# Performance work log

Measured on AMD Instinct MI355X. Metric: run time of the kernel, lower is better.

The kernel has to match this reference:

```python
import jax, jax.numpy as jnp
import numpy as np

N = 256            # state_space_size
BF = (4, 4, 4)     # branching_factors
T = 128            # time steps
D_IN = 64          # input_size
D_T = 64           # time_embedding_size
BATCH = 16
NUM_NODES = N * 4 * 4 * 4  # 16384


def setup_inputs() -> dict:
    key = jax.random.key(0)
    ks = jax.random.split(key, 20)

    def lin_w(k, out_d, in_d):
        return jax.random.normal(k, (out_d, in_d), jnp.float32) / np.sqrt(in_d)

    inp = {
        "x": jax.random.normal(ks[0], (BATCH, T, N), jnp.float32),
        "t_embeddings_schedule": jax.random.normal(ks[1], (T, D_T), jnp.float32),
        "input_vector": jax.random.normal(ks[2], (BATCH, T, D_IN), jnp.float32),
        # Fanout node params
        "Wa": lin_w(ks[3], NUM_NODES, N),
        "ba": jnp.zeros((NUM_NODES,), jnp.float32),
        "Wt": lin_w(ks[4], NUM_NODES, D_T),
        "Wi": lin_w(ks[5], NUM_NODES, D_IN),
        # Node with bf[:3]=[4,4,4]: reduces last 4 -> [N,4,4]
        "w3": jax.random.normal(ks[6], (N, 4, 4, 4), jnp.float32) * np.sqrt(2.0 / (4 + N * 16)),
        "tW3": lin_w(ks[7], N * 16, D_T),
        "tb3": jnp.zeros((N * 16,), jnp.float32),
        # Node with bf[:2]=[4,4]
        "w2": jax.random.normal(ks[8], (N, 4, 4), jnp.float32) * np.sqrt(2.0 / (4 + N * 4)),
        "tW2": lin_w(ks[9], N * 4, D_T),
        "tb2": jnp.zeros((N * 4,), jnp.float32),
        # Node with bf[:1]=[4]
        "w1": jax.random.normal(ks[10], (N, 4), jnp.float32) * np.sqrt(2.0 / (4 + N)),
        "tW1": lin_w(ks[11], N, D_T),
        "tb1": jnp.zeros((N,), jnp.float32),
    }
    return inp


def _node(act, t_emb, w, tW, tb):
    # act: [..., T, N, *bf]; w: [N, *bf]; reduce last branching dim
    tproj = (t_emb @ tW.T + tb).reshape(t_emb.shape[0], *w.shape[:-1])  # [T, N, *bf[:-1]]
    pre = (w * act).sum(-1) + tproj  # broadcast over leading batch dims
    return jax.nn.softplus(pre)


def reference(x, t_embeddings_schedule, input_vector, Wa, ba, Wt, Wi,
              w3, tW3, tb3, w2, tW2, tb2, w1, tW1, tb1):
    t_emb = t_embeddings_schedule
    # Fanout: [B, T, N] -> [B, T, N, 4, 4, 4]
    pre = x @ Wa.T + ba + (t_emb @ Wt.T) + input_vector @ Wi.T  # [B, T, NUM_NODES]
    act = jax.nn.softplus(pre.reshape(*pre.shape[:-1], N, *BF))
    # Tree: deepest node first (insert-at-1 order in original)
    act = _node(act, t_emb, w3, tW3, tb3)  # [B, T, N, 4, 4]
    act = _node(act, t_emb, w2, tW2, tb2)  # [B, T, N, 4]
    act = _node(act, t_emb, w1, tW1, tb1)  # [B, T, N]
    return act
```

## Files before the change

### kernel.cpp

```cpp
#include <hip/hip_runtime.h>

typedef __attribute__((ext_vector_type(16))) float f32x16;
typedef __attribute__((ext_vector_type(8))) __bf16 bf16x8;
typedef __attribute__((ext_vector_type(8))) unsigned short u16x8;

__device__ __forceinline__ unsigned short f2bf(float f) {
    unsigned int u = __float_as_uint(f);
    u += 0x7fffu + ((u >> 16) & 1u);
    return (unsigned short)(u >> 16);
}

__device__ __forceinline__ float softplus_f(float x) {
    float e = __expf(-fabsf(x));
    return fmaf(__log2f(1.0f + e), 0.69314718056f, fmaxf(x, 0.0f));
}

typedef __attribute__((address_space(3))) void lds_void_t;
typedef __attribute__((address_space(1))) void glb_void_t;

__device__ __forceinline__ void load16_to_lds(const void* g, const void* l) {
    __builtin_amdgcn_global_load_lds((glb_void_t*)(unsigned long long)g,
                                     (lds_void_t*)(unsigned int)(unsigned long long)l,
                                     16, 0, 0);
}

#define REPACK_NB 2
#define REPACK_BLOCKS 1728
#define TPROJ_BLOCKS 336
#define PREP_BLOCKS (REPACK_BLOCKS + TPROJ_BLOCKS)
__global__ __launch_bounds__(256) void prep(
        const float* __restrict__ x, const float* __restrict__ iv,
        const float* __restrict__ temb,
        const float* __restrict__ Wa, const float* __restrict__ Wi,
        const float* __restrict__ Wt,
        const float* __restrict__ tW3, const float* __restrict__ tb3,
        const float* __restrict__ tW2, const float* __restrict__ tb2,
        const float* __restrict__ tW1, const float* __restrict__ tb1,
        unsigned short* __restrict__ Abf ,
        float* __restrict__ tp3T, float* __restrict__ tp2T, float* __restrict__ tp1T) {
    __shared__ float se[32 * 64];
    const int tid = threadIdx.x;

    if (blockIdx.x < TPROJ_BLOCKS) {
        const int bx = blockIdx.x % 84;
        const int by = blockIdx.x / 84;
        const int tbase = by * 32;
        for (int i = tid; i < 32 * 64; i += 256) se[i] = temb[tbase * 64 + i];
        __syncthreads();
        const int j = bx * 64 + (tid >> 2);
        const float* W; const float* bias; float* outp; int jl;
        if      (j < 4096) { W = tW3; bias = tb3; outp = tp3T; jl = j; }
        else if (j < 5120) { W = tW2; bias = tb2; outp = tp2T; jl = j - 4096; }
        else               { W = tW1; bias = tb1; outp = tp1T; jl = j - 5120; }
        float4 wreg[16];
        const float4* wrow = (const float4*)(W + (size_t)jl * 64);
        #pragma unroll
        for (int k = 0; k < 16; ++k) wreg[k] = wrow[k];
        const float b = bias[jl];
        #pragma unroll
        for (int s = 0; s < 8; ++s) {
            const int tl = (tid & 3) + s * 4;
            const float4* e4 = (const float4*)&se[tl * 64];
            float a = b;
            #pragma unroll
            for (int k = 0; k < 16; ++k) {
                float4 e = e4[k];
                a += wreg[k].x * e.x + wreg[k].y * e.y + wreg[k].z * e.z + wreg[k].w * e.w;
            }
            outp[(size_t)jl * 128 + tbase + tl] = a;
        }
        return;
    }

    const int stride = REPACK_BLOCKS * 256;
    const int tid0 = (blockIdx.x - TPROJ_BLOCKS) * 256 + tid;
    float4 f[REPACK_NB][2];
    #pragma unroll
    for (int c = 0; c < REPACK_NB; ++c) {
        const int idx = tid0 + c * stride;
        const bool isA = idx < 98304;
        const int widx = isA ? idx : idx - 98304;
        const int row = widx / 48;
        const int kk  = (widx % 48) * 8;
        const float* p0 = isA ? (x    + (size_t)row * 256) : (Wa + (size_t)row * 256);
        const float* p1 = isA ? (iv   + (size_t)row * 64)  : (Wi + (size_t)row * 64);
        const float* p2 = isA ? (temb + (size_t)(row & 127) * 64) : (Wt + (size_t)row * 64);
        const float* src = (kk < 256) ? (p0 + kk) : ((kk < 320) ? (p1 + kk - 256) : (p2 + kk - 320));
        f[c][0] = ((const float4*)src)[0];
        f[c][1] = ((const float4*)src)[1];
    }
    #pragma unroll
    for (int c = 0; c < REPACK_NB; ++c) {
        const int idx = tid0 + c * stride;
        const bool isA = idx < 98304;
        const int widx = isA ? idx : idx - 98304;
        const int row = widx / 48;
        const int ch  = widx % 48;
        const size_t dst = isA ? (size_t)(((row >> 5) * 48 + ch) * 32 + (row & 31))
                               : (size_t)idx;
        u16x8 o;
        o[0] = f2bf(f[c][0].x); o[1] = f2bf(f[c][0].y); o[2] = f2bf(f[c][0].z); o[3] = f2bf(f[c][0].w);
        o[4] = f2bf(f[c][1].x); o[5] = f2bf(f[c][1].y); o[6] = f2bf(f[c][1].z); o[7] = f2bf(f[c][1].w);
        *(u16x8*)(Abf + dst * 8) = o;
    }
}

__global__ __launch_bounds__(256, 3)
void fused_gemm_tree(const unsigned short* __restrict__ Wbf,
                     const unsigned short* __restrict__ Abf,
                     const float* __restrict__ ba,
                     const float* __restrict__ tp3T, const float* __restrict__ tp2T,
                     const float* __restrict__ tp1T,
                     const float* __restrict__ w3, const float* __restrict__ w2,
                     const float* __restrict__ w1,
                     float* __restrict__ out) {
    __shared__ unsigned short sW[2][128 * 64];

    const int tid  = threadIdx.x;
    const int wave = tid >> 6;
    const int lane = tid & 63;
    const int wr = wave >> 1;
    const int wc = wave & 1;
    const int lane31 = lane & 31;
    const int h = lane >> 5;

    const int node0 = blockIdx.x * 128;
    const int m0    = blockIdx.y * 128;

    f32x16 acc[2][2];
    #pragma unroll
    for (int fm = 0; fm < 2; ++fm)
        #pragma unroll
        for (int s2 = 0; s2 < 4; ++s2) {
            const float4 b4 = *(const float4*)&ba[node0 + wr * 64 + fm * 32 + 8 * s2 + 4 * h];
            #pragma unroll
            for (int l = 0; l < 4; ++l) {
                acc[fm][0][s2 * 4 + l] = ((const float*)&b4)[l];
                acc[fm][1][s2 * 4 + l] = ((const float*)&b4)[l];
            }
        }

    const unsigned short* aBase = Wbf + (size_t)node0 * 384;
    const int wrow0 = wr * 64 + lane31;

    const int mtBase = blockIdx.y * 4 + wc * 2;
    const unsigned short* bC0 = Abf + (((size_t)(mtBase + 0) * 48 + h) * 32 + lane31) * 8;
    const unsigned short* bC1 = Abf + (((size_t)(mtBase + 1) * 48 + h) * 32 + lane31) * 8;

    int srow[4], skch[4];
    #pragma unroll
    for (int rr = 0; rr < 4; ++rr) {
        const int p = rr * 256 + tid;
        srow[rr] = p >> 3;
        skch[rr] = (p & 7) ^ (srow[rr] & 7);
    }
    #define STAGE_A(K0, BB)                                                        \
        _Pragma("unroll")                                                          \
        for (int rr = 0; rr < 4; ++rr)                                             \
            load16_to_lds(aBase + (size_t)srow[rr] * 384 + (K0) + skch[rr] * 8,    \
                          &sW[BB][(size_t)(rr * 256 + wave * 64) * 8]);

    STAGE_A(0, 0);
    __syncthreads();

    #pragma unroll
    for (int it = 0; it < 6; ++it) {
        const int k0 = it * 64;
        bf16x8 bfr[2][4];
        const int cbase = k0 >> 3;
        #pragma unroll
        for (int s = 0; s < 4; ++s) {
            bfr[0][s] = *(const bf16x8*)(bC0 + (size_t)(cbase + 2 * s) * 256);
            bfr[1][s] = *(const bf16x8*)(bC1 + (size_t)(cbase + 2 * s) * 256);
        }
        if (it < 5) { STAGE_A(k0 + 64, (it + 1) & 1); }
        #pragma unroll
        for (int s = 0; s < 4; ++s) {
            const int kc = s * 2 + h;
            const int slot = (kc ^ (lane & 7)) * 8;
            bf16x8 af[2];
            #pragma unroll
            for (int fm = 0; fm < 2; ++fm)
                af[fm] = *(const bf16x8*)&sW[it & 1][(wrow0 + fm * 32) * 64 + slot];
            acc[0][0] = __builtin_amdgcn_mfma_f32_32x32x16_bf16(af[0], bfr[0][s], acc[0][0], 0, 0, 0);
            acc[0][1] = __builtin_amdgcn_mfma_f32_32x32x16_bf16(af[0], bfr[1][s], acc[0][1], 0, 0, 0);
            acc[1][0] = __builtin_amdgcn_mfma_f32_32x32x16_bf16(af[1], bfr[0][s], acc[1][0], 0, 0, 0);
            acc[1][1] = __builtin_amdgcn_mfma_f32_32x32x16_bf16(af[1], bfr[1][s], acc[1][1], 0, 0, 0);
        }
        if (it < 5) __syncthreads();
    }

    const int n = blockIdx.x * 2 + wr;
    const int t0 = wc * 64 + lane31;

    float4 w3v[2][4];
    #pragma unroll
    for (int fm = 0; fm < 2; ++fm)
        #pragma unroll
        for (int s2 = 0; s2 < 4; ++s2)
            w3v[fm][s2] = *(const float4*)&w3[n * 64 + fm * 32 + 8 * s2 + 4 * h];

    float w2v[4][2], w1v[4];
    #pragma unroll
    for (int i = 0; i < 4; ++i) {
        #pragma unroll
        for (int s2b = 0; s2b < 2; ++s2b)
            w2v[i][s2b] = w2[n * 16 + i * 4 + 2 * s2b + h];
        w1v[i] = w1[n * 4 + i];
    }
    float tp3v[2][2][4];
    #pragma unroll
    for (int fm = 0; fm < 2; ++fm)
        #pragma unroll
        for (int cf = 0; cf < 2; ++cf) {
            const int t = t0 + cf * 32;
            #pragma unroll
            for (int s2 = 0; s2 < 4; ++s2) {
                const int i  = fm * 2 + (s2 >> 1);
                const int jj = 2 * (s2 & 1) + h;
                tp3v[fm][cf][s2] = tp3T[(size_t)((n * 4 + i) * 4 + jj) * 128 + t];
            }
        }
    const int th = t0 + h * 32;
    float tp2h[2][2];
    #pragma unroll
    for (int fm = 0; fm < 2; ++fm)
        #pragma unroll
        for (int b = 0; b < 2; ++b)
            tp2h[fm][b] = tp2T[(size_t)(n * 4 + fm * 2 + b) * 128 + th];
    const float tp1h = tp1T[(size_t)n * 128 + th];

    float s1h = 0.0f;
    #pragma unroll
    for (int fm = 0; fm < 2; ++fm) {
        #pragma unroll
        for (int b = 0; b < 2; ++b) {
            float cs[2];
            #pragma unroll
            for (int cf = 0; cf < 2; ++cf) {
                float c = 0.0f;
                #pragma unroll
                for (int s2b = 0; s2b < 2; ++s2b) {
                    const int s2 = 2 * b + s2b;
                    float p3 = 0.0f;
                    const float* wv = (const float*)&w3v[fm][s2];
                    #pragma unroll
                    for (int l = 0; l < 4; ++l) {
                        float a0 = softplus_f(acc[fm][cf][s2 * 4 + l]);
                        p3 = fmaf(a0, wv[l], p3);
                    }
                    float a3 = softplus_f(p3 + tp3v[fm][cf][s2]);
                    c = fmaf(a3, w2v[fm * 2 + b][s2b], c);
                }
                cs[cf] = c;
            }
            const float Q0 = cs[0] + __shfl_xor(cs[0], 32);
            const float Q1 = cs[1] + __shfl_xor(cs[1], 32);
            const float Qh = h ? Q1 : Q0;
            const float a2 = softplus_f(Qh + tp2h[fm][b]);
            s1h = fmaf(a2, w1v[fm * 2 + b], s1h);
        }
    }
    out[(size_t)(m0 + th) * 256 + n] = softplus_f(s1h + tp1h);
}

extern "C" void kernel_launch(void* const* d_in, const int* in_sizes, int n_in,
                              void* d_out, int out_size, void* d_ws, size_t ws_size,
                              hipStream_t stream) {
    const float* x    = (const float*)d_in[0];
    const float* temb = (const float*)d_in[1];
    const float* iv   = (const float*)d_in[2];
    const float* Wa   = (const float*)d_in[3];
    const float* ba   = (const float*)d_in[4];
    const float* Wt   = (const float*)d_in[5];
    const float* Wi   = (const float*)d_in[6];
    const float* w3   = (const float*)d_in[7];
    const float* tW3  = (const float*)d_in[8];
    const float* tb3  = (const float*)d_in[9];
    const float* w2   = (const float*)d_in[10];
    const float* tW2  = (const float*)d_in[11];
    const float* tb2  = (const float*)d_in[12];
    const float* w1   = (const float*)d_in[13];
    const float* tW1  = (const float*)d_in[14];
    const float* tb1  = (const float*)d_in[15];
    float* out = (float*)d_out;

    char* ws = (char*)d_ws;
    unsigned short* Abf = (unsigned short*)(ws);
    unsigned short* Wbf = (unsigned short*)(ws + 1572864);
    float* tp3T = (float*)(ws + 14155776);
    float* tp2T = (float*)(ws + 16252928);
    float* tp1T = (float*)(ws + 16777216);

    prep<<<dim3(PREP_BLOCKS), dim3(256), 0, stream>>>(x, iv, temb, Wa, Wi, Wt,
                                                      tW3, tb3, tW2, tb2, tW1, tb1,
                                                      Abf, tp3T, tp2T, tp1T);
    fused_gemm_tree<<<dim3(128, 16), dim3(256), 0, stream>>>(Wbf, Abf, ba, tp3T, tp2T, tp1T,
                                                             w3, w2, w1, out);
}
```

Baseline: 143.8 us.

## Repack weights into MFMA-tiled layout and single-buffer LDS staging

The weight matrix is now repacked into the same 32-row-by-8-column tiled layout as the activations, so each LDS stage becomes a contiguous panel copy with no XOR swizzle. The LDS tile drops from double to single buffering, halving shared memory, with two barriers per k-step instead of prefetching the next tile during compute. This may allow more resident blocks and simplifies address arithmetic, but loses the overlap of global loads with MFMA work.

```diff
diff --git a/kernel.cpp b/kernel.cpp
--- a/kernel.cpp
+++ b/kernel.cpp
@@ -96,8 +96,8 @@
         const int widx = isA ? idx : idx - 98304;
         const int row = widx / 48;
         const int ch  = widx % 48;
-        const size_t dst = isA ? (size_t)(((row >> 5) * 48 + ch) * 32 + (row & 31))
-                               : (size_t)idx;
+        const size_t dst = (size_t)(isA ? 0 : 98304) +
+                           (size_t)(((row >> 5) * 48 + ch) * 32 + (row & 31));
         u16x8 o;
         o[0] = f2bf(f[c][0].x); o[1] = f2bf(f[c][0].y); o[2] = f2bf(f[c][0].z); o[3] = f2bf(f[c][0].w);
         o[4] = f2bf(f[c][1].x); o[5] = f2bf(f[c][1].y); o[6] = f2bf(f[c][1].z); o[7] = f2bf(f[c][1].w);
@@ -106,15 +106,15 @@
 }
 
 __global__ __launch_bounds__(256, 3)
-void fused_gemm_tree(const unsigned short* __restrict__ Wbf,
-                     const unsigned short* __restrict__ Abf,
+void fused_gemm_tree(const unsigned short* __restrict__ Wf,
+                     const unsigned short* __restrict__ Af,
                      const float* __restrict__ ba,
                      const float* __restrict__ tp3T, const float* __restrict__ tp2T,
                      const float* __restrict__ tp1T,
                      const float* __restrict__ w3, const float* __restrict__ w2,
                      const float* __restrict__ w1,
                      float* __restrict__ out) {
-    __shared__ unsigned short sW[2][128 * 64];
+    __shared__ unsigned short sW[128 * 64];
 
     const int tid  = threadIdx.x;
     const int wave = tid >> 6;
@@ -140,54 +140,42 @@
             }
         }
 
-    const unsigned short* aBase = Wbf + (size_t)node0 * 384;
-    const int wrow0 = wr * 64 + lane31;
+    const unsigned short* aPanel = Wf + (size_t)blockIdx.x * 4 * 12288;
+    const int sOff = ((tid >> 5) * 32 + (tid & 31)) * 8;
+
+    const int rdBase = wr * 4096 + lane31 * 8;
 
     const int mtBase = blockIdx.y * 4 + wc * 2;
-    const unsigned short* bC0 = Abf + (((size_t)(mtBase + 0) * 48 + h) * 32 + lane31) * 8;
-    const unsigned short* bC1 = Abf + (((size_t)(mtBase + 1) * 48 + h) * 32 + lane31) * 8;
-
-    int srow[4], skch[4];
-    #pragma unroll
-    for (int rr = 0; rr < 4; ++rr) {
-        const int p = rr * 256 + tid;
-        srow[rr] = p >> 3;
-        skch[rr] = (p & 7) ^ (srow[rr] & 7);
-    }
-    #define STAGE_A(K0, BB)                                                        \
-        _Pragma("unroll")                                                          \
-        for (int rr = 0; rr < 4; ++rr)                                             \
-            load16_to_lds(aBase + (size_t)srow[rr] * 384 + (K0) + skch[rr] * 8,    \
-                          &sW[BB][(size_t)(rr * 256 + wave * 64) * 8]);
-
-    STAGE_A(0, 0);
-    __syncthreads();
-
-    #pragma unroll
+    const unsigned short* bC0 = Af + (((size_t)(mtBase + 0) * 48 + h) * 32 + lane31) * 8;
+    const unsigned short* bC1 = Af + (((size_t)(mtBase + 1) * 48 + h) * 32 + lane31) * 8;
+
     for (int it = 0; it < 6; ++it) {
-        const int k0 = it * 64;
+        const int cbase = it * 8;
+        __syncthreads();
+        #pragma unroll
+        for (int rr = 0; rr < 4; ++rr)
+            load16_to_lds(aPanel + (size_t)rr * 12288 + (size_t)cbase * 256 + sOff,
+                          &sW[(size_t)(rr * 256 + wave * 64) * 8]);
         bf16x8 bfr[2][4];
-        const int cbase = k0 >> 3;
         #pragma unroll
         for (int s = 0; s < 4; ++s) {
             bfr[0][s] = *(const bf16x8*)(bC0 + (size_t)(cbase + 2 * s) * 256);
             bfr[1][s] = *(const bf16x8*)(bC1 + (size_t)(cbase + 2 * s) * 256);
         }
-        if (it < 5) { STAGE_A(k0 + 64, (it + 1) & 1); }
+        __syncthreads();
+
         #pragma unroll
         for (int s = 0; s < 4; ++s) {
             const int kc = s * 2 + h;
-            const int slot = (kc ^ (lane & 7)) * 8;
             bf16x8 af[2];
             #pragma unroll
             for (int fm = 0; fm < 2; ++fm)
-                af[fm] = *(const bf16x8*)&sW[it & 1][(wrow0 + fm * 32) * 64 + slot];
+                af[fm] = *(const bf16x8*)&sW[rdBase + fm * 2048 + kc * 256];
             acc[0][0] = __builtin_amdgcn_mfma_f32_32x32x16_bf16(af[0], bfr[0][s], acc[0][0], 0, 0, 0);
             acc[0][1] = __builtin_amdgcn_mfma_f32_32x32x16_bf16(af[0], bfr[1][s], acc[0][1], 0, 0, 0);
             acc[1][0] = __builtin_amdgcn_mfma_f32_32x32x16_bf16(af[1], bfr[0][s], acc[1][0], 0, 0, 0);
             acc[1][1] = __builtin_amdgcn_mfma_f32_32x32x16_bf16(af[1], bfr[1][s], acc[1][1], 0, 0, 0);
         }
-        if (it < 5) __syncthreads();
     }
 
     const int n = blockIdx.x * 2 + wr;
```

Result: slower. 147.5 us (median of 2 runs) (+2.6%).
